# Performance work log

Measured on AMD Instinct MI355X. Metric: run time of the kernel, lower is better.

The kernel has to match this reference:

```python
import jax, jax.numpy as jnp
import numpy as np

K = 32  # top-k along the feature dim


def setup_inputs() -> dict:
    key = jax.random.key(0)
    B, S, D = 8, 4096, 1024
    x = jax.random.normal(key, (B, S, D), dtype=jnp.float32)
    return {
        "x": x,
        "log_alpha": jnp.zeros((), dtype=jnp.float32),
        "log_sigma": jnp.zeros((), dtype=jnp.float32),
        "ema_mean": jnp.zeros((D,), dtype=jnp.float32),
        "ema_sq": jnp.ones((D,), dtype=jnp.float32),
    }


def reference(x, log_alpha, log_sigma, ema_mean, ema_sq):
    # base = exact (erf) GELU, matching torch.nn.GELU default
    base = jax.nn.gelu(x, approximate=False)
    # per-channel z-score using EMA stats
    ema_var = jnp.clip(ema_sq - ema_mean ** 2, 1e-6, None)
    z_abs = jnp.abs(x - ema_mean) * jax.lax.rsqrt(ema_var)  # [B,S,D]
    # surprise = mean of top-K |z| along feature dim
    top_vals, _ = jax.lax.top_k(z_abs, K)                    # [B,S,K]
    surp = jnp.mean(top_vals, axis=-1, keepdims=True)        # [B,S,1]
    gate = 1.0 + jnp.exp(log_alpha) * jnp.tanh(jnp.exp(log_sigma) * surp)
    return base * gate
```

## Files before the change

### kernel.cpp

```cpp
#include <hip/hip_runtime.h>
#include <math.h>

#define D 1024
#define TOPK 32
#define VPT 16
#define WPB 4

typedef float vfloat4 __attribute__((ext_vector_type(4)));

__device__ __forceinline__ float waveMax(float v) {
#pragma unroll
  for (int off = 32; off >= 1; off >>= 1)
    v = fmaxf(v, __shfl_xor(v, off, 64));
  return v;
}
__device__ __forceinline__ float waveSumF(float v) {
#pragma unroll
  for (int off = 32; off >= 1; off >>= 1)
    v += __shfl_xor(v, off, 64);
  return v;
}

__device__ __forceinline__ float fast_gelu(float x) {
  const float x2 = x * x;
  const float p = __builtin_fmaf(0.044715f, x2, 1.0f);
  const float a = -1.5957691216f * x * p;
  const float e = __expf(a);
  const float r = __builtin_amdgcn_rcpf(1.0f + e);
  return x * r;
}

__global__ __launch_bounds__(256) void prep_stats(const float* __restrict__ ema_mean,
                                                  const float* __restrict__ ema_sq,
                                                  float* __restrict__ inv_std) {
  int i = blockIdx.x * 256 + threadIdx.x;
  if (i < D) {
    float m = ema_mean[i];
    float v = ema_sq[i] - m * m;
    inv_std[i] = rsqrtf(fmaxf(v, 1e-6f));
  }
}

__global__ __launch_bounds__(256, 4) void gelu_gate(const float* __restrict__ x,
                                                    const float* __restrict__ p_la,
                                                    const float* __restrict__ p_ls,
                                                    const float* __restrict__ ema_mean,
                                                    const float* __restrict__ inv_std,
                                                    float* __restrict__ out,
                                                    int n_rows) {
  const int wave = threadIdx.x >> 6;
  const int lane = threadIdx.x & 63;
  const int row = blockIdx.x * WPB + wave;
  if (row >= n_rows) return;
  const float* __restrict__ xr = x + (size_t)row * D;
  float* __restrict__ orow = out + (size_t)row * D;

  float xv[VPT], za[VPT];
#pragma unroll
  for (int j = 0; j < 4; ++j) {
    const int c = j * 256 + lane * 4;
    const float4 xx = *reinterpret_cast<const float4*>(xr + c);
    const float4 mm = *reinterpret_cast<const float4*>(ema_mean + c);
    const float4 ss = *reinterpret_cast<const float4*>(inv_std + c);
    xv[4 * j + 0] = xx.x; xv[4 * j + 1] = xx.y;
    xv[4 * j + 2] = xx.z; xv[4 * j + 3] = xx.w;
    za[4 * j + 0] = fabsf(xx.x - mm.x) * ss.x;
    za[4 * j + 1] = fabsf(xx.y - mm.y) * ss.y;
    za[4 * j + 2] = fabsf(xx.z - mm.z) * ss.z;
    za[4 * j + 3] = fabsf(xx.w - mm.w) * ss.w;
  }

  float m = 0.0f;
#pragma unroll
  for (int i = 0; i < VPT; ++i) m = fmaxf(m, za[i]);
  m = waveMax(m);

  float lo = 0.0f;
  float hi = __uint_as_float(__float_as_uint(m) + 1u);
  for (;;) {
    const float mid = 0.5f * (lo + hi);
    if (!(mid > lo) || !(mid < hi)) break;
    int c = 0;
#pragma unroll
    for (int i = 0; i < VPT; ++i)
      c += (int)__popcll(__ballot(za[i] >= mid));
    if (c >= TOPK) {
      lo = mid;
      if (c == TOPK) break;
    } else {
      hi = mid;
    }
  }
  const float t = lo;

  float s = 0.0f;
  int cg = 0;
#pragma unroll
  for (int i = 0; i < VPT; ++i) {
    const bool g = za[i] > t;
    s += g ? za[i] : 0.0f;
    cg += (int)__popcll(__ballot(g));
  }
  s = waveSumF(s);
  const float topsum = s + (float)(TOPK - cg) * t;
  const float surp = topsum * (1.0f / (float)TOPK);
  const float gate = 1.0f + expf(p_la[0]) * tanhf(expf(p_ls[0]) * surp);

#pragma unroll
  for (int j = 0; j < 4; ++j) {
    const int c = j * 256 + lane * 4;
    vfloat4 o;
    o.x = fast_gelu(xv[4 * j + 0]) * gate;
    o.y = fast_gelu(xv[4 * j + 1]) * gate;
    o.z = fast_gelu(xv[4 * j + 2]) * gate;
    o.w = fast_gelu(xv[4 * j + 3]) * gate;
    __builtin_nontemporal_store(o, reinterpret_cast<vfloat4*>(orow + c));
  }
}

extern "C" void kernel_launch(void* const* d_in, const int* in_sizes, int n_in,
                              void* d_out, int out_size, void* d_ws, size_t ws_size,
                              hipStream_t stream) {
  const float* x    = (const float*)d_in[0];
  const float* la   = (const float*)d_in[1];
  const float* ls   = (const float*)d_in[2];
  const float* mean = (const float*)d_in[3];
  const float* sq   = (const float*)d_in[4];
  float* out = (float*)d_out;
  float* inv_std = (float*)d_ws;

  const int n = in_sizes[0];
  const int n_rows = n / D;

  prep_stats<<<(D + 255) / 256, 256, 0, stream>>>(mean, sq, inv_std);

  const int grid = (n_rows + WPB - 1) / WPB;
  gelu_gate<<<grid, WPB * 64, 0, stream>>>(x, la, ls, mean, inv_std, out, n_rows);
}
```

Baseline: 239.0 us.

## Process two rows per wave with fixed-iteration interleaved threshold search

Each wave now handles two rows, loading both up front and interleaving their ballot-based threshold searches to raise memory-level and instruction-level parallelism. The exact-converging bisection is replaced by a fixed 8-iteration bisection with count correction, removing data-dependent loop trip counts. The exp of the gate parameters is precomputed in the prep kernel, and tanh uses a fast exp-based form. A fixed 8-step search can leave a coarse threshold, so the top-k sum becomes approximate when several values sit near the cutoff, and register pressure roughly doubles.

```diff
diff --git a/kernel.cpp b/kernel.cpp
--- a/kernel.cpp
+++ b/kernel.cpp
@@ -4,22 +4,11 @@
 #define D 1024
 #define TOPK 32
 #define VPT 16
+#define RPW 2
 #define WPB 4
+#define BITER 8
 
 typedef float vfloat4 __attribute__((ext_vector_type(4)));
-
-__device__ __forceinline__ float waveMax(float v) {
-#pragma unroll
-  for (int off = 32; off >= 1; off >>= 1)
-    v = fmaxf(v, __shfl_xor(v, off, 64));
-  return v;
-}
-__device__ __forceinline__ float waveSumF(float v) {
-#pragma unroll
-  for (int off = 32; off >= 1; off >>= 1)
-    v += __shfl_xor(v, off, 64);
-  return v;
-}
 
 __device__ __forceinline__ float fast_gelu(float x) {
   const float x2 = x * x;
@@ -30,91 +19,139 @@
   return x * r;
 }
 
+__device__ __forceinline__ float fast_tanh_pos(float y) {
+  const float e = __expf(-2.0f * y);
+  return (1.0f - e) * __builtin_amdgcn_rcpf(1.0f + e);
+}
+
 __global__ __launch_bounds__(256) void prep_stats(const float* __restrict__ ema_mean,
                                                   const float* __restrict__ ema_sq,
-                                                  float* __restrict__ inv_std) {
+                                                  const float* __restrict__ p_la,
+                                                  const float* __restrict__ p_ls,
+                                                  float* __restrict__ ws) {
   int i = blockIdx.x * 256 + threadIdx.x;
   if (i < D) {
     float m = ema_mean[i];
     float v = ema_sq[i] - m * m;
-    inv_std[i] = rsqrtf(fmaxf(v, 1e-6f));
+    ws[i] = rsqrtf(fmaxf(v, 1e-6f));
+  }
+  if (i == 0) {
+    ws[D] = expf(p_la[0]);
+    ws[D + 1] = expf(p_ls[0]);
   }
 }
 
 __global__ __launch_bounds__(256, 4) void gelu_gate(const float* __restrict__ x,
-                                                    const float* __restrict__ p_la,
-                                                    const float* __restrict__ p_ls,
                                                     const float* __restrict__ ema_mean,
-                                                    const float* __restrict__ inv_std,
+                                                    const float* __restrict__ ws,
                                                     float* __restrict__ out,
                                                     int n_rows) {
   const int wave = threadIdx.x >> 6;
   const int lane = threadIdx.x & 63;
-  const int row = blockIdx.x * WPB + wave;
-  if (row >= n_rows) return;
-  const float* __restrict__ xr = x + (size_t)row * D;
-  float* __restrict__ orow = out + (size_t)row * D;
+  const int row0 = (blockIdx.x * WPB + wave) * RPW;
+  if (row0 >= n_rows) return;
+  const bool has1 = (row0 + 1) < n_rows;
+  const float* __restrict__ xr0 = x + (size_t)row0 * D;
+  const float* __restrict__ xr1 = xr0 + (has1 ? D : 0);
 
-  float xv[VPT], za[VPT];
+  float4 a0[4], a1[4];
+#pragma unroll
+  for (int j = 0; j < 4; ++j)
+    a0[j] = *reinterpret_cast<const float4*>(xr0 + j * 256 + lane * 4);
+#pragma unroll
+  for (int j = 0; j < 4; ++j)
+    a1[j] = *reinterpret_cast<const float4*>(xr1 + j * 256 + lane * 4);
+
+  float za0[VPT], za1[VPT];
 #pragma unroll
   for (int j = 0; j < 4; ++j) {
     const int c = j * 256 + lane * 4;
-    const float4 xx = *reinterpret_cast<const float4*>(xr + c);
     const float4 mm = *reinterpret_cast<const float4*>(ema_mean + c);
-    const float4 ss = *reinterpret_cast<const float4*>(inv_std + c);
-    xv[4 * j + 0] = xx.x; xv[4 * j + 1] = xx.y;
-    xv[4 * j + 2] = xx.z; xv[4 * j + 3] = xx.w;
-    za[4 * j + 0] = fabsf(xx.x - mm.x) * ss.x;
-    za[4 * j + 1] = fabsf(xx.y - mm.y) * ss.y;
-    za[4 * j + 2] = fabsf(xx.z - mm.z) * ss.z;
-    za[4 * j + 3] = fabsf(xx.w - mm.w) * ss.w;
+    const float4 ss = *reinterpret_cast<const float4*>(ws + c);
+    za0[4 * j + 0] = fabsf(a0[j].x - mm.x) * ss.x;
+    za0[4 * j + 1] = fabsf(a0[j].y - mm.y) * ss.y;
+    za0[4 * j + 2] = fabsf(a0[j].z - mm.z) * ss.z;
+    za0[4 * j + 3] = fabsf(a0[j].w - mm.w) * ss.w;
+    za1[4 * j + 0] = fabsf(a1[j].x - mm.x) * ss.x;
+    za1[4 * j + 1] = fabsf(a1[j].y - mm.y) * ss.y;
+    za1[4 * j + 2] = fabsf(a1[j].z - mm.z) * ss.z;
+    za1[4 * j + 3] = fabsf(a1[j].w - mm.w) * ss.w;
   }
 
-  float m = 0.0f;
-#pragma unroll
-  for (int i = 0; i < VPT; ++i) m = fmaxf(m, za[i]);
-  m = waveMax(m);
-
-  float lo = 0.0f;
-  float hi = __uint_as_float(__float_as_uint(m) + 1u);
-  for (;;) {
-    const float mid = 0.5f * (lo + hi);
-    if (!(mid > lo) || !(mid < hi)) break;
-    int c = 0;
-#pragma unroll
-    for (int i = 0; i < VPT; ++i)
-      c += (int)__popcll(__ballot(za[i] >= mid));
-    if (c >= TOPK) {
-      lo = mid;
-      if (c == TOPK) break;
-    } else {
-      hi = mid;
-    }
-  }
-  const float t = lo;
-
-  float s = 0.0f;
-  int cg = 0;
+  float m0 = 0.0f, m1 = 0.0f;
 #pragma unroll
   for (int i = 0; i < VPT; ++i) {
-    const bool g = za[i] > t;
-    s += g ? za[i] : 0.0f;
-    cg += (int)__popcll(__ballot(g));
+    m0 = fmaxf(m0, za0[i]);
+    m1 = fmaxf(m1, za1[i]);
   }
-  s = waveSumF(s);
-  const float topsum = s + (float)(TOPK - cg) * t;
-  const float surp = topsum * (1.0f / (float)TOPK);
-  const float gate = 1.0f + expf(p_la[0]) * tanhf(expf(p_ls[0]) * surp);
+#pragma unroll
+  for (int off = 32; off >= 1; off >>= 1) {
+    m0 = fmaxf(m0, __shfl_xor(m0, off, 64));
+    m1 = fmaxf(m1, __shfl_xor(m1, off, 64));
+  }
 
+  float lo0 = 0.0f, hi0 = __uint_as_float(__float_as_uint(m0) + 1u);
+  float lo1 = 0.0f, hi1 = __uint_as_float(__float_as_uint(m1) + 1u);
+  int clo0 = D, clo1 = D;
+#pragma unroll
+  for (int it = 0; it < BITER; ++it) {
+    const float mid0 = 0.5f * (lo0 + hi0);
+    const float mid1 = 0.5f * (lo1 + hi1);
+    int c0 = 0, c1 = 0;
+#pragma unroll
+    for (int i = 0; i < VPT; ++i) {
+      c0 += (int)__popcll(__ballot(za0[i] >= mid0));
+      c1 += (int)__popcll(__ballot(za1[i] >= mid1));
+    }
+    const bool g0 = (c0 >= TOPK);
+    const bool g1 = (c1 >= TOPK);
+    lo0 = g0 ? mid0 : lo0;  hi0 = g0 ? hi0 : mid0;  clo0 = g0 ? c0 : clo0;
+    lo1 = g1 ? mid1 : lo1;  hi1 = g1 ? hi1 : mid1;  clo1 = g1 ? c1 : clo1;
+  }
+
+  const float t0 = lo0, t1 = lo1;
+  float s0 = 0.0f, s1 = 0.0f;
+#pragma unroll
+  for (int i = 0; i < VPT; ++i) {
+    s0 += (za0[i] >= t0) ? za0[i] : 0.0f;
+    s1 += (za1[i] >= t1) ? za1[i] : 0.0f;
+  }
+#pragma unroll
+  for (int off = 32; off >= 1; off >>= 1) {
+    s0 += __shfl_xor(s0, off, 64);
+    s1 += __shfl_xor(s1, off, 64);
+  }
+  const float top0 = s0 - (float)(clo0 - TOPK) * t0;
+  const float top1 = s1 - (float)(clo1 - TOPK) * t1;
+
+  const float alpha = ws[D];
+  const float sigma = ws[D + 1];
+  const float gate0 = 1.0f + alpha * fast_tanh_pos(sigma * (top0 * (1.0f / (float)TOPK)));
+  const float gate1 = 1.0f + alpha * fast_tanh_pos(sigma * (top1 * (1.0f / (float)TOPK)));
+
+  float* __restrict__ o0 = out + (size_t)row0 * D;
+  float* __restrict__ o1 = o0 + D;
 #pragma unroll
   for (int j = 0; j < 4; ++j) {
     const int c = j * 256 + lane * 4;
-    vfloat4 o;
-    o.x = fast_gelu(xv[4 * j + 0]) * gate;
-    o.y = fast_gelu(xv[4 * j + 1]) * gate;
-    o.z = fast_gelu(xv[4 * j + 2]) * gate;
-    o.w = fast_gelu(xv[4 * j + 3]) * gate;
-    __builtin_nontemporal_store(o, reinterpret_cast<vfloat4*>(orow + c));
+    vfloat4 v0;
+    v0.x = fast_gelu(a0[j].x) * gate0;
+    v0.y = fast_gelu(a0[j].y) * gate0;
+    v0.z = fast_gelu(a0[j].z) * gate0;
+    v0.w = fast_gelu(a0[j].w) * gate0;
+    __builtin_nontemporal_store(v0, reinterpret_cast<vfloat4*>(o0 + c));
+  }
+  if (has1) {
+#pragma unroll
+    for (int j = 0; j < 4; ++j) {
+      const int c = j * 256 + lane * 4;
+      vfloat4 v1;
+      v1.x = fast_gelu(a1[j].x) * gate1;
+      v1.y = fast_gelu(a1[j].y) * gate1;
+      v1.z = fast_gelu(a1[j].z) * gate1;
+      v1.w = fast_gelu(a1[j].w) * gate1;
+      __builtin_nontemporal_store(v1, reinterpret_cast<vfloat4*>(o1 + c));
+    }
   }
 }
 
@@ -127,13 +164,14 @@
   const float* mean = (const float*)d_in[3];
   const float* sq   = (const float*)d_in[4];
   float* out = (float*)d_out;
-  float* inv_std = (float*)d_ws;
+  float* ws = (float*)d_ws;
 
   const int n = in_sizes[0];
   const int n_rows = n / D;
 
-  prep_stats<<<(D + 255) / 256, 256, 0, stream>>>(mean, sq, inv_std);
+  prep_stats<<<(D + 255) / 256, 256, 0, stream>>>(mean, sq, la, ls, ws);
 
-  const int grid = (n_rows + WPB - 1) / WPB;
-  gelu_gate<<<grid, WPB * 64, 0, stream>>>(x, la, ls, mean, inv_std, out, n_rows);
+  const int rows_per_block = WPB * RPW;
+  const int grid = (n_rows + rows_per_block - 1) / rows_per_block;
+  gelu_gate<<<grid, WPB * 64, 0, stream>>>(x, mean, ws, out, n_rows);
 }
```

After: 239.4 us. Within noise of the previous version (+0.2%).
